# Performance work log

Hardware: AMD Instinct MI355X
Metric: run time of the kernel (lower is better)

## Reference

```python
import jax, jax.numpy as jnp
import numpy as np

N_NODES = 100000
N_EDGES = 2400000
IN_DIM = 128
HID = 32


def setup_inputs() -> dict:
    key = jax.random.key(0)
    ks = jax.random.split(key, 6)
    x = jax.random.normal(ks[0], (N_NODES, IN_DIM), dtype=jnp.float32)
    edge_index = jax.random.randint(ks[1], (2, N_EDGES), 0, N_NODES, dtype=jnp.int64)
    # Glorot-style scaled weights
    W1 = jax.random.normal(ks[2], (IN_DIM, HID), dtype=jnp.float32) / np.sqrt(IN_DIM)
    W2 = jax.random.normal(ks[3], (HID, HID), dtype=jnp.float32) / np.sqrt(HID)
    W3 = jax.random.normal(ks[4], (HID, 1), dtype=jnp.float32) / np.sqrt(HID)
    b1 = jnp.zeros((HID,), jnp.float32)
    b2 = jnp.zeros((HID,), jnp.float32)
    b3 = jnp.zeros((1,), jnp.float32)
    return {"x": x, "edge_index": edge_index, "W1": W1, "b1": b1,
            "W2": W2, "b2": b2, "W3": W3, "b3": b3}


def reference(x, edge_index, W1, b1, W2, b2, W3, b3):
    N = x.shape[0]
    # GCNConv default: add self-loops, symmetric deg^-1/2 normalization.
    loop = jnp.arange(N, dtype=edge_index.dtype)
    row = jnp.concatenate([edge_index[0], loop])  # message source (x_j)
    col = jnp.concatenate([edge_index[1], loop])  # aggregation target
    deg = jax.ops.segment_sum(jnp.ones_like(col, dtype=x.dtype), col, num_segments=N)
    dinv = jnp.where(deg > 0, jax.lax.rsqrt(deg), 0.0)
    norm = dinv[row] * dinv[col]  # [E+N]

    def gcn(h, W, b):
        h = h @ W                              # transform first (PyG GCNConv)
        msg = h[row] * norm[:, None]           # gather + normalize
        return jax.ops.segment_sum(msg, col, num_segments=N) + b  # scatter-add

    h = jax.nn.relu(gcn(x, W1, b1))
    h = jax.nn.relu(gcn(h, W2, b2))
    return gcn(h, W3, b3)  # [N, 1]
```

## Files before the change

kernel.cpp:

```cpp
#include <hip/hip_runtime.h>
#include <hip/hip_fp16.h>

#define IN_DIM 128
#define HID    32
#define CHUNK  6144
#define EPT    12
#define BSH    9
#define BSIZE  512
#define CAPSH  14
#define ROWBITS 17
#define STRIDE 5

typedef union { float2 f2; __half2 h2[2]; } hpack;

__global__ void k_init_cursor(int* __restrict__ cursor) {
    cursor[threadIdx.x] = threadIdx.x << CAPSH;
}


__global__ __launch_bounds__(512) void k_fusedA(const int* __restrict__ row,
                                                const int* __restrict__ col,
                                                int* __restrict__ cursor,
                                                int* __restrict__ bpack,
                                                const float* __restrict__ x,
                                                const float* __restrict__ W1,
                                                float* __restrict__ T0,
                                                int E, int N, int gBuild) {
    __shared__ __align__(16) char smem[34816];
    int tid = threadIdx.x;

    int b = blockIdx.x;
    int q = b / STRIDE, r = b % STRIDE;
    bool isSort = (r == 0) && (q < gBuild);

    if (isSort) {
        int* lh   = (int*)smem;
        int* ls   = lh + 256;
        int* gdst = ls + 256;
        int* sp   = gdst + 256;
        unsigned char* sb = (unsigned char*)(sp + CHUNK);

        if (tid < 256) lh[tid] = 0;
        __syncthreads();

        int base = q * CHUNK;
        int nE = min(CHUNK, E - base);
        int e0 = tid * EPT;
        int m  = min(EPT, nE - e0);

        int ecol[EPT], erow[EPT], rk[EPT];
        if (m == EPT) {
            int4 ca = *(const int4*)(col + base + e0);
            int4 cb = *(const int4*)(col + base + e0 + 4);
            int4 cc = *(const int4*)(col + base + e0 + 8);
            int4 ra = *(const int4*)(row + base + e0);
            int4 rb = *(const int4*)(row + base + e0 + 4);
            int4 rc = *(const int4*)(row + base + e0 + 8);
            ecol[0]=ca.x; ecol[1]=ca.y; ecol[2]=ca.z;  ecol[3]=ca.w;
            ecol[4]=cb.x; ecol[5]=cb.y; ecol[6]=cb.z;  ecol[7]=cb.w;
            ecol[8]=cc.x; ecol[9]=cc.y; ecol[10]=cc.z; ecol[11]=cc.w;
            erow[0]=ra.x; erow[1]=ra.y; erow[2]=ra.z;  erow[3]=ra.w;
            erow[4]=rb.x; erow[5]=rb.y; erow[6]=rb.z;  erow[7]=rb.w;
            erow[8]=rc.x; erow[9]=rc.y; erow[10]=rc.z; erow[11]=rc.w;
        } else {
            for (int j = 0; j < m; ++j) {
                ecol[j] = col[base + e0 + j];
                erow[j] = row[base + e0 + j];
            }
        }

        for (int j = 0; j < m; ++j)
            rk[j] = atomicAdd(&lh[ecol[j] >> BSH], 1);
        __syncthreads();

        int v = 0;
        if (tid < 256) { v = lh[tid]; ls[tid] = v; }
        __syncthreads();
        for (int off = 1; off < 256; off <<= 1) {
            int nv = 0;
            if (tid < 256) nv = ls[tid] + (tid >= off ? ls[tid - off] : 0);
            __syncthreads();
            if (tid < 256) ls[tid] = nv;
            __syncthreads();
        }
        if (tid < 256) ls[tid] -= v;
        __syncthreads();

        if (tid < 256) {
            int bb = (tid + q) & 255;
            int vb = lh[bb];
            if (vb) gdst[bb] = atomicAdd(&cursor[bb], vb) - ls[bb];
        }
        __syncthreads();

        for (int j = 0; j < m; ++j) {
            int c = ecol[j];
            int bk = c >> BSH;
            int idx = ls[bk] + rk[j];
            sp[idx] = ((c & (BSIZE - 1)) << ROWBITS) | erow[j];
            sb[idx] = (unsigned char)bk;
        }
        __syncthreads();

        for (int i = tid; i < nE; i += 512) {
            int bk = sb[i];
            bpack[gdst[bk] + i] = sp[i];
        }
    } else {
        int xIdx = b - min(q + (r > 0 ? 1 : 0), gBuild);

        float* lw = (float*)smem;
        for (int i = tid; i < IN_DIM * HID; i += 512) lw[i] = W1[i];
        __syncthreads();

        int lane = tid & 7;
        int jb = lane * 4;
        int n  = xIdx * 64 + (tid >> 3);
        if (n >= N) return;

        const float* xr = x + (size_t)n * IN_DIM;
        float a0 = 0.f, a1 = 0.f, a2 = 0.f, a3 = 0.f;
        #pragma unroll 8
        for (int k = 0; k < IN_DIM; ++k) {
            float xv = xr[k];
            const float* wp = &lw[k * HID + jb];
            a0 = fmaf(xv, wp[0], a0);
            a1 = fmaf(xv, wp[1], a1);
            a2 = fmaf(xv, wp[2], a2);
            a3 = fmaf(xv, wp[3], a3);
        }
        hpack u;
        u.h2[0] = __floats2half2_rn(a0, a1);
        u.h2[1] = __floats2half2_rn(a2, a3);
        ((float2*)T0)[(size_t)n * 8 + lane] = u.f2;
    }
}


__global__ __launch_bounds__(1024) void kC_fill(const int* __restrict__ bpack,
                                                const int* __restrict__ cursor,
                                                int* __restrict__ csr,
                                                int* __restrict__ rowptr,
                                                int* __restrict__ deg,
                                                float* __restrict__ dinv,
                                                float* __restrict__ B0, int N) {
    __shared__ int cnt[BSIZE], ex[BSIZE], c2[BSIZE];
    __shared__ int sp[1 << CAPSH];
    int tid = threadIdx.x;
    int b = blockIdx.x;
    int s = b << CAPSH;
    int ne = cursor[b] - s;
    int c0 = b << BSH;

    if (tid < BSIZE) { cnt[tid] = 0; c2[tid] = 0; }
    __syncthreads();

    for (int i = tid; i < ne; i += 1024) {
        int v = bpack[s + i];
        sp[i] = v;
        atomicAdd(&cnt[v >> ROWBITS], 1);
    }
    __syncthreads();

    if (tid < BSIZE) ex[tid] = cnt[tid];
    __syncthreads();
    for (int off = 1; off < BSIZE; off <<= 1) {
        int nv = 0;
        if (tid < BSIZE) nv = ex[tid] + (tid >= off ? ex[tid - off] : 0);
        __syncthreads();
        if (tid < BSIZE) ex[tid] = nv;
        __syncthreads();
    }

    if (tid < BSIZE) {
        int ev = ex[tid] - cnt[tid];
        ex[tid] = ev;
        int n = c0 + tid;
        if (n < N) {
            rowptr[n] = s + ev;
            deg[n]    = cnt[tid];
            dinv[n]   = rsqrtf((float)cnt[tid] + 1.0f);
        }
    }
    __syncthreads();

    for (int i = tid; i < ne; i += 1024) {
        int v = sp[i];
        int c = v >> ROWBITS;
        int k = atomicAdd(&c2[c], 1);
        csr[s + ex[c] + k] = v & ((1 << ROWBITS) - 1);
    }

    for (int j = tid; j < BSIZE * 4; j += 1024) {
        int nl = j >> 2;
        int n = c0 + nl;
        if (n < N) {
            float dv = rsqrtf((float)cnt[nl] + 1.0f);
            union { float4 f4; __half2 h2[4]; } u;
            u.f4 = ((const float4*)B0)[(size_t)n * 4 + (j & 3)];
            #pragma unroll
            for (int qq = 0; qq < 4; ++qq) {
                float2 f = __half22float2(u.h2[qq]);
                u.h2[qq] = __floats2half2_rn(f.x * dv, f.y * dv);
            }
            ((float4*)B0)[(size_t)n * 4 + (j & 3)] = u.f4;
        }
    }
}


#define GLOAD(i, r) hpack p##i; p##i.f2 = B2[(size_t)(r) * 8 + lane]
#define GACC(i) { float2 a = __half22float2(p##i.h2[0]), b = __half22float2(p##i.h2[1]); \
                  acc.x += a.x; acc.y += a.y; acc.z += b.x; acc.w += b.y; }

__global__ __launch_bounds__(256) void k_gxf2(const int* __restrict__ rowptr,
                                              const int* __restrict__ deg,
                                              const int* __restrict__ csr,
                                              const float* __restrict__ Bin,
                                              const float* __restrict__ dinv,
                                              const float* __restrict__ bias,
                                              const float* __restrict__ W2,
                                              float* __restrict__ Bout, int N) {
    __shared__ float lw[HID * HID];
    for (int i = threadIdx.x; i < HID * HID; i += 256) lw[i] = W2[i];
    __syncthreads();

    int lane = threadIdx.x & 7;
    int jb = lane * 4;
    int n  = blockIdx.x * 32 + (threadIdx.x >> 3);
    if (n >= N) return;

    const float2* B2 = (const float2*)Bin;
    hpack u0; u0.f2 = B2[(size_t)n * 8 + lane];
    float2 l0 = __half22float2(u0.h2[0]);
    float2 l1 = __half22float2(u0.h2[1]);
    float4 acc = make_float4(l0.x, l0.y, l1.x, l1.y);

    int s = rowptr[n], cnt = deg[n];
    int k = 0;
    for (; k + 7 < cnt; k += 8) {
        int r0 = csr[s+k],   r1 = csr[s+k+1], r2 = csr[s+k+2], r3 = csr[s+k+3];
        int r4 = csr[s+k+4], r5 = csr[s+k+5], r6 = csr[s+k+6], r7 = csr[s+k+7];
        GLOAD(0, r0); GLOAD(1, r1); GLOAD(2, r2); GLOAD(3, r3);
        GLOAD(4, r4); GLOAD(5, r5); GLOAD(6, r6); GLOAD(7, r7);
        GACC(0); GACC(1); GACC(2); GACC(3); GACC(4); GACC(5); GACC(6); GACC(7);
    }
    for (; k + 3 < cnt; k += 4) {
        int r0 = csr[s+k], r1 = csr[s+k+1], r2 = csr[s+k+2], r3 = csr[s+k+3];
        GLOAD(0, r0); GLOAD(1, r1); GLOAD(2, r2); GLOAD(3, r3);
        GACC(0); GACC(1); GACC(2); GACC(3);
    }
    for (; k < cnt; ++k) {
        GLOAD(0, csr[s+k]); GACC(0);
    }
    float dv = dinv[n];
    float4 b4 = ((const float4*)bias)[lane];
    float4 o;
    o.x = fmaxf(fmaf(dv, acc.x, b4.x), 0.f);
    o.y = fmaxf(fmaf(dv, acc.y, b4.y), 0.f);
    o.z = fmaxf(fmaf(dv, acc.z, b4.z), 0.f);
    o.w = fmaxf(fmaf(dv, acc.w, b4.w), 0.f);

    float t0 = 0.f, t1 = 0.f, t2 = 0.f, t3 = 0.f;
    #pragma unroll
    for (int sl = 0; sl < 8; ++sl) {
        float h0 = __shfl(o.x, sl, 8);
        float h1 = __shfl(o.y, sl, 8);
        float h2 = __shfl(o.z, sl, 8);
        float h3 = __shfl(o.w, sl, 8);
        const float* w0 = &lw[(sl * 4 + 0) * HID + jb];
        const float* w1 = &lw[(sl * 4 + 1) * HID + jb];
        const float* w2 = &lw[(sl * 4 + 2) * HID + jb];
        const float* w3 = &lw[(sl * 4 + 3) * HID + jb];
        t0 = fmaf(h0, w0[0], t0); t1 = fmaf(h0, w0[1], t1);
        t2 = fmaf(h0, w0[2], t2); t3 = fmaf(h0, w0[3], t3);
        t0 = fmaf(h1, w1[0], t0); t1 = fmaf(h1, w1[1], t1);
        t2 = fmaf(h1, w1[2], t2); t3 = fmaf(h1, w1[3], t3);
        t0 = fmaf(h2, w2[0], t0); t1 = fmaf(h2, w2[1], t1);
        t2 = fmaf(h2, w2[2], t2); t3 = fmaf(h2, w2[3], t3);
        t0 = fmaf(h3, w3[0], t0); t1 = fmaf(h3, w3[1], t1);
        t2 = fmaf(h3, w3[2], t2); t3 = fmaf(h3, w3[3], t3);
    }
    hpack w;
    w.h2[0] = __floats2half2_rn(t0 * dv, t1 * dv);
    w.h2[1] = __floats2half2_rn(t2 * dv, t3 * dv);
    ((float2*)Bout)[(size_t)n * 8 + lane] = w.f2;
}

__global__ __launch_bounds__(256) void k_gxf3(const int* __restrict__ rowptr,
                                              const int* __restrict__ deg,
                                              const int* __restrict__ csr,
                                              const float* __restrict__ Bin,
                                              const float* __restrict__ dinv,
                                              const float* __restrict__ bias,
                                              const float* __restrict__ W3,
                                              float* __restrict__ s3, int N) {
    __shared__ float lw[HID];
    if (threadIdx.x < HID) lw[threadIdx.x] = W3[threadIdx.x];
    __syncthreads();

    int lane = threadIdx.x & 7;
    int jb = lane * 4;
    int n  = blockIdx.x * 32 + (threadIdx.x >> 3);
    if (n >= N) return;

    const float2* B2 = (const float2*)Bin;
    hpack u0; u0.f2 = B2[(size_t)n * 8 + lane];
    float2 l0 = __half22float2(u0.h2[0]);
    float2 l1 = __half22float2(u0.h2[1]);
    float4 acc = make_float4(l0.x, l0.y, l1.x, l1.y);

    int s = rowptr[n], cnt = deg[n];
    int k = 0;
    for (; k + 7 < cnt; k += 8) {
        int r0 = csr[s+k],   r1 = csr[s+k+1], r2 = csr[s+k+2], r3 = csr[s+k+3];
        int r4 = csr[s+k+4], r5 = csr[s+k+5], r6 = csr[s+k+6], r7 = csr[s+k+7];
        GLOAD(0, r0); GLOAD(1, r1); GLOAD(2, r2); GLOAD(3, r3);
        GLOAD(4, r4); GLOAD(5, r5); GLOAD(6, r6); GLOAD(7, r7);
        GACC(0); GACC(1); GACC(2); GACC(3); GACC(4); GACC(5); GACC(6); GACC(7);
    }
    for (; k + 3 < cnt; k += 4) {
        int r0 = csr[s+k], r1 = csr[s+k+1], r2 = csr[s+k+2], r3 = csr[s+k+3];
        GLOAD(0, r0); GLOAD(1, r1); GLOAD(2, r2); GLOAD(3, r3);
        GACC(0); GACC(1); GACC(2); GACC(3);
    }
    for (; k < cnt; ++k) {
        GLOAD(0, csr[s+k]); GACC(0);
    }
    float dv = dinv[n];
    float4 b4 = ((const float4*)bias)[lane];
    float4 o;
    o.x = fmaxf(fmaf(dv, acc.x, b4.x), 0.f);
    o.y = fmaxf(fmaf(dv, acc.y, b4.y), 0.f);
    o.z = fmaxf(fmaf(dv, acc.z, b4.z), 0.f);
    o.w = fmaxf(fmaf(dv, acc.w, b4.w), 0.f);

    float p = o.x * lw[jb] + o.y * lw[jb + 1] + o.z * lw[jb + 2] + o.w * lw[jb + 3];
    p += __shfl_xor(p, 1, 8);
    p += __shfl_xor(p, 2, 8);
    p += __shfl_xor(p, 4, 8);
    if (lane == 0) s3[n] = p * dv;
}

__global__ __launch_bounds__(256) void k_gather1(const int* __restrict__ rowptr,
                                                 const int* __restrict__ deg,
                                                 const int* __restrict__ csr,
                                                 const float* __restrict__ s3,
                                                 const float* __restrict__ dinv,
                                                 const float* __restrict__ b3,
                                                 float* __restrict__ out, int N) {
    int lane = threadIdx.x & 7;
    int n    = blockIdx.x * 32 + (threadIdx.x >> 3);
    if (n >= N) return;

    int s = rowptr[n], cnt = deg[n];
    float acc = 0.f;
    for (int k = lane; k < cnt; k += 8) acc += s3[csr[s + k]];
    acc += __shfl_xor(acc, 1, 8);
    acc += __shfl_xor(acc, 2, 8);
    acc += __shfl_xor(acc, 4, 8);
    if (lane == 0) out[n] = fmaf(dinv[n], acc + s3[n], b3[0]);
}


static inline size_t align64(size_t x) { return (x + 63) & ~(size_t)63; }

extern "C" void kernel_launch(void* const* d_in, const int* in_sizes, int n_in,
                              void* d_out, int out_size, void* d_ws, size_t ws_size,
                              hipStream_t stream) {
    const float* x   = (const float*)d_in[0];
    const int*   ei  = (const int*)d_in[1];
    const float* W1  = (const float*)d_in[2];
    const float* b1  = (const float*)d_in[3];
    const float* W2  = (const float*)d_in[4];
    const float* b2  = (const float*)d_in[5];
    const float* W3  = (const float*)d_in[6];
    const float* b3  = (const float*)d_in[7];

    const int N = in_sizes[0] / IN_DIM;
    const int E = in_sizes[1] / 2;
    const int* row = ei;
    const int* col = ei + E;

    const int NB = (N + BSIZE - 1) / BSIZE;
    const size_t bktCap = (size_t)NB << CAPSH;

    char* p = (char*)d_ws;
    size_t off = 0;
    float* dinv   = (float*)(p + off); off = align64(off + (size_t)N * 4);
    float* B0     = (float*)(p + off); off = align64(off + (size_t)N * HID * 2);
    float* B1     = (float*)(p + off); off = align64(off + (size_t)N * HID * 2);
    float* s3     = (float*)(p + off); off = align64(off + (size_t)N * 4);
    int*   deg    = (int*)  (p + off); off = align64(off + (size_t)N * 4);
    int*   rowptr = (int*)  (p + off); off = align64(off + (size_t)N * 4);
    int*   cursor = (int*)  (p + off); off = align64(off + 256 * 4);
    int*   bpack  = (int*)  (p + off); off = align64(off + bktCap * 4);
    int*   csr    = (int*)  (p + off); off = align64(off + bktCap * 4);
    float* out    = (float*)d_out;

    const int gBuild = (E + CHUNK - 1) / CHUNK;
    const int gX64   = (N + 63) / 64;
    const int gNode  = (N + 31) / 32;

    k_init_cursor<<<1, 256, 0, stream>>>(cursor);
    k_fusedA<<<gBuild + gX64, 512, 0, stream>>>(row, col, cursor, bpack, x, W1, B0, E, N, gBuild);
    kC_fill <<<NB, 1024, 0, stream>>>(bpack, cursor, csr, rowptr, deg, dinv, B0, N);

    k_gxf2   <<<gNode, 256, 0, stream>>>(rowptr, deg, csr, B0, dinv, b1, W2, B1, N);
    k_gxf3   <<<gNode, 256, 0, stream>>>(rowptr, deg, csr, B1, dinv, b2, W3, s3, N);
    k_gather1<<<gNode, 256, 0, stream>>>(rowptr, deg, csr, s3, dinv, b3, out, N);
}
```

Measured before the change: 130.5 us.

## Sort nodes by degree within each bucket and vectorize x loads in transform

The CSR build kernel now computes a per-bucket counting sort of nodes by in-degree (capped at 127) and writes a permutation array. All three aggregation kernels map warps onto nodes through this order, so the 8-lane groups in a wavefront handle nodes of similar degree and waste fewer cycles on divergent loop trip counts. Separately, the x@W1 loop now reads x with float4 loads instead of scalar loads. The cost is an extra scan in kC_fill, one indirection per node, and less locality in the per-node output writes.

```diff
diff --git a/kernel.cpp b/kernel.cpp
--- a/kernel.cpp
+++ b/kernel.cpp
@@ -118,16 +118,23 @@
         int n  = xIdx * 64 + (tid >> 3);
         if (n >= N) return;
 
-        const float* xr = x + (size_t)n * IN_DIM;
+        const float4* xr4 = (const float4*)(x + (size_t)n * IN_DIM);
         float a0 = 0.f, a1 = 0.f, a2 = 0.f, a3 = 0.f;
         #pragma unroll 8
-        for (int k = 0; k < IN_DIM; ++k) {
-            float xv = xr[k];
-            const float* wp = &lw[k * HID + jb];
-            a0 = fmaf(xv, wp[0], a0);
-            a1 = fmaf(xv, wp[1], a1);
-            a2 = fmaf(xv, wp[2], a2);
-            a3 = fmaf(xv, wp[3], a3);
+        for (int kq = 0; kq < IN_DIM / 4; ++kq) {
+            float4 v = xr4[kq];
+            const float* w0 = &lw[(kq * 4 + 0) * HID + jb];
+            const float* w1 = &lw[(kq * 4 + 1) * HID + jb];
+            const float* w2 = &lw[(kq * 4 + 2) * HID + jb];
+            const float* w3 = &lw[(kq * 4 + 3) * HID + jb];
+            a0 = fmaf(v.x, w0[0], a0); a1 = fmaf(v.x, w0[1], a1);
+            a2 = fmaf(v.x, w0[2], a2); a3 = fmaf(v.x, w0[3], a3);
+            a0 = fmaf(v.y, w1[0], a0); a1 = fmaf(v.y, w1[1], a1);
+            a2 = fmaf(v.y, w1[2], a2); a3 = fmaf(v.y, w1[3], a3);
+            a0 = fmaf(v.z, w2[0], a0); a1 = fmaf(v.z, w2[1], a1);
+            a2 = fmaf(v.z, w2[2], a2); a3 = fmaf(v.z, w2[3], a3);
+            a0 = fmaf(v.w, w3[0], a0); a1 = fmaf(v.w, w3[1], a1);
+            a2 = fmaf(v.w, w3[2], a2); a3 = fmaf(v.w, w3[3], a3);
         }
         hpack u;
         u.h2[0] = __floats2half2_rn(a0, a1);
@@ -143,8 +150,10 @@
                                                 int* __restrict__ rowptr,
                                                 int* __restrict__ deg,
                                                 float* __restrict__ dinv,
-                                                float* __restrict__ B0, int N) {
+                                                float* __restrict__ B0,
+                                                int* __restrict__ order, int N) {
     __shared__ int cnt[BSIZE], ex[BSIZE], c2[BSIZE];
+    __shared__ int dh[128], dex[128];
     __shared__ int sp[1 << CAPSH];
     int tid = threadIdx.x;
     int b = blockIdx.x;
@@ -153,6 +162,7 @@
     int c0 = b << BSH;
 
     if (tid < BSIZE) { cnt[tid] = 0; c2[tid] = 0; }
+    if (tid < 128) dh[tid] = 0;
     __syncthreads();
 
     for (int i = tid; i < ne; i += 1024) {
@@ -172,6 +182,7 @@
         __syncthreads();
     }
 
+    int mybin = -1, myrank = 0;
     if (tid < BSIZE) {
         int ev = ex[tid] - cnt[tid];
         ex[tid] = ev;
@@ -180,9 +191,23 @@
             rowptr[n] = s + ev;
             deg[n]    = cnt[tid];
             dinv[n]   = rsqrtf((float)cnt[tid] + 1.0f);
-        }
-    }
-    __syncthreads();
+            mybin = min(cnt[tid], 127);
+            myrank = atomicAdd(&dh[mybin], 1);
+        }
+    }
+    __syncthreads();
+
+    if (tid < 128) dex[tid] = dh[tid];
+    __syncthreads();
+    for (int off = 1; off < 128; off <<= 1) {
+        int nv = 0;
+        if (tid < 128) nv = dex[tid] + (tid >= off ? dex[tid - off] : 0);
+        __syncthreads();
+        if (tid < 128) dex[tid] = nv;
+        __syncthreads();
+    }
+    if (mybin >= 0)
+        order[c0 + dex[mybin] - dh[mybin] + myrank] = c0 + tid;
 
     for (int i = tid; i < ne; i += 1024) {
         int v = sp[i];
@@ -216,6 +241,7 @@
 __global__ __launch_bounds__(256) void k_gxf2(const int* __restrict__ rowptr,
                                               const int* __restrict__ deg,
                                               const int* __restrict__ csr,
+                                              const int* __restrict__ order,
                                               const float* __restrict__ Bin,
                                               const float* __restrict__ dinv,
                                               const float* __restrict__ bias,
@@ -227,8 +253,9 @@
 
     int lane = threadIdx.x & 7;
     int jb = lane * 4;
-    int n  = blockIdx.x * 32 + (threadIdx.x >> 3);
-    if (n >= N) return;
+    int g  = blockIdx.x * 32 + (threadIdx.x >> 3);
+    if (g >= N) return;
+    int n = order[g];
 
     const float2* B2 = (const float2*)Bin;
     hpack u0; u0.f2 = B2[(size_t)n * 8 + lane];
@@ -290,6 +317,7 @@
 __global__ __launch_bounds__(256) void k_gxf3(const int* __restrict__ rowptr,
                                               const int* __restrict__ deg,
                                               const int* __restrict__ csr,
+                                              const int* __restrict__ order,
                                               const float* __restrict__ Bin,
                                               const float* __restrict__ dinv,
                                               const float* __restrict__ bias,
@@ -301,8 +329,9 @@
 
     int lane = threadIdx.x & 7;
     int jb = lane * 4;
-    int n  = blockIdx.x * 32 + (threadIdx.x >> 3);
-    if (n >= N) return;
+    int g  = blockIdx.x * 32 + (threadIdx.x >> 3);
+    if (g >= N) return;
+    int n = order[g];
 
     const float2* B2 = (const float2*)Bin;
     hpack u0; u0.f2 = B2[(size_t)n * 8 + lane];
@@ -345,13 +374,15 @@
 __global__ __launch_bounds__(256) void k_gather1(const int* __restrict__ rowptr,
                                                  const int* __restrict__ deg,
                                                  const int* __restrict__ csr,
+                                                 const int* __restrict__ order,
                                                  const float* __restrict__ s3,
                                                  const float* __restrict__ dinv,
                                                  const float* __restrict__ b3,
                                                  float* __restrict__ out, int N) {
     int lane = threadIdx.x & 7;
-    int n    = blockIdx.x * 32 + (threadIdx.x >> 3);
-    if (n >= N) return;
+    int g    = blockIdx.x * 32 + (threadIdx.x >> 3);
+    if (g >= N) return;
+    int n = order[g];
 
     int s = rowptr[n], cnt = deg[n];
     float acc = 0.f;
@@ -393,6 +424,7 @@
     float* s3     = (float*)(p + off); off = align64(off + (size_t)N * 4);
     int*   deg    = (int*)  (p + off); off = align64(off + (size_t)N * 4);
     int*   rowptr = (int*)  (p + off); off = align64(off + (size_t)N * 4);
+    int*   order  = (int*)  (p + off); off = align64(off + (size_t)N * 4);
     int*   cursor = (int*)  (p + off); off = align64(off + 256 * 4);
     int*   bpack  = (int*)  (p + off); off = align64(off + bktCap * 4);
     int*   csr    = (int*)  (p + off); off = align64(off + bktCap * 4);
@@ -404,9 +436,9 @@
 
     k_init_cursor<<<1, 256, 0, stream>>>(cursor);
     k_fusedA<<<gBuild + gX64, 512, 0, stream>>>(row, col, cursor, bpack, x, W1, B0, E, N, gBuild);
-    kC_fill <<<NB, 1024, 0, stream>>>(bpack, cursor, csr, rowptr, deg, dinv, B0, N);
-
-    k_gxf2   <<<gNode, 256, 0, stream>>>(rowptr, deg, csr, B0, dinv, b1, W2, B1, N);
-    k_gxf3   <<<gNode, 256, 0, stream>>>(rowptr, deg, csr, B1, dinv, b2, W3, s3, N);
-    k_gather1<<<gNode, 256, 0, stream>>>(rowptr, deg, csr, s3, dinv, b3, out, N);
-}
+    kC_fill <<<NB, 1024, 0, stream>>>(bpack, cursor, csr, rowptr, deg, dinv, B0, order, N);
+
+    k_gxf2   <<<gNode, 256, 0, stream>>>(rowptr, deg, csr, order, B0, dinv, b1, W2, B1, N);
+    k_gxf3   <<<gNode, 256, 0, stream>>>(rowptr, deg, csr, order, B1, dinv, b2, W3, s3, N);
+    k_gather1<<<gNode, 256, 0, stream>>>(rowptr, deg, csr, order, s3, dinv, b3, out, N);
+}
```

Result: slower. 150.9 us (+15.6%).
